# Optimization experiments

Measured on AMD Instinct MI355X. Metric: run time of the kernel, lower is better.

The kernel has to match this reference:

```python
import jax, jax.numpy as jnp
import numpy as np

B = 4        # number of point clouds (equal-sized, batch ids are sorted blocks)
K = 3        # knn_interpolate k
EPS_D = 1e-16
EPS_BN = 1e-5


def setup_inputs() -> dict:
    key = jax.random.key(0)
    ks = jax.random.split(key, 12)
    N_src, N_tgt = 2048, 8192
    C, C_skip = 256, 128
    x = jax.random.normal(ks[0], (B * N_src, C), dtype=jnp.float32)
    pos = jax.random.normal(ks[1], (B * N_src, 3), dtype=jnp.float32)
    x_skip = jax.random.normal(ks[2], (B * N_tgt, C_skip), dtype=jnp.float32)
    pos_skip = jax.random.normal(ks[3], (B * N_tgt, 3), dtype=jnp.float32)
    batch = jnp.repeat(jnp.arange(B, dtype=jnp.int64), N_src)
    batch_skip = jnp.repeat(jnp.arange(B, dtype=jnp.int64), N_tgt)
    d_in = C + C_skip  # 384
    W1 = jax.random.normal(ks[4], (d_in, 256), dtype=jnp.float32) / np.sqrt(d_in)
    b1 = jnp.zeros((256,), dtype=jnp.float32)
    g1 = jnp.ones((256,), dtype=jnp.float32)
    be1 = jnp.zeros((256,), dtype=jnp.float32)
    W2 = jax.random.normal(ks[5], (256, 256), dtype=jnp.float32) / 16.0
    b2 = jnp.zeros((256,), dtype=jnp.float32)
    g2 = jnp.ones((256,), dtype=jnp.float32)
    be2 = jnp.zeros((256,), dtype=jnp.float32)
    return dict(x=x, pos=pos, batch=batch, x_skip=x_skip, pos_skip=pos_skip,
                batch_skip=batch_skip, W1=W1, b1=b1, g1=g1, be1=be1,
                W2=W2, b2=b2, g2=g2, be2=be2)


def _knn_interpolate(x, pos, pos_skip):
    # equal-size clouds: reshape instead of per-batch masking
    C = x.shape[1]
    N = pos.shape[0] // B
    M = pos_skip.shape[0] // B
    ps = pos.reshape(B, N, 3)
    pt = pos_skip.reshape(B, M, 3)
    # squared distances [B, M, N] via |a|^2 + |b|^2 - 2ab
    d2 = (jnp.sum(pt * pt, -1)[:, :, None]
          + jnp.sum(ps * ps, -1)[:, None, :]
          - 2.0 * jnp.einsum('bmd,bnd->bmn', pt, ps))
    neg_d2, idx = jax.lax.top_k(-d2, K)            # idx: [B, M, K]
    w = 1.0 / jnp.maximum(-neg_d2, EPS_D)          # inverse squared distance
    xf = x.reshape(B, N, C)
    feats = xf[jnp.arange(B)[:, None, None], idx]  # [B, M, K, C] irregular gather
    y = jnp.sum(feats * w[..., None], axis=2) / jnp.sum(w, axis=2)[..., None]
    return y.reshape(B * M, C)


def _mlp_block(h, W, b, g, be):
    h = jnp.maximum(h @ W + b, 0.0)                # Linear + ReLU
    mu = jnp.mean(h, axis=0)
    var = jnp.mean((h - mu) ** 2, axis=0)          # biased var (torch BN training)
    return g * (h - mu) / jnp.sqrt(var + EPS_BN) + be


def reference(x, pos, batch, x_skip, pos_skip, batch_skip,
              W1, b1, g1, be1, W2, b2, g2, be2):
    y = _knn_interpolate(x, pos, pos_skip)
    h = jnp.concatenate([y, x_skip], axis=1)       # [B*M, 384]
    h = _mlp_block(h, W1, b1, g1, be1)
    h = _mlp_block(h, W2, b2, g2, be2)
    return h
```

## Files before the change

kernel.cpp:

```cpp
#include <hip/hip_runtime.h>
#include <hip/hip_bf16.h>

typedef __attribute__((ext_vector_type(8))) short short8;
typedef __attribute__((ext_vector_type(4))) short s16x4;
typedef __attribute__((ext_vector_type(4))) int   i32x4;
typedef __attribute__((ext_vector_type(4))) float f32x4;
typedef __attribute__((ext_vector_type(2))) float f32x2;
typedef __attribute__((ext_vector_type(8))) float f32x8;

constexpr int BATCH  = 4;
constexpr int NSRC   = 2048;
constexpr int NTGT   = 8192;
constexpr int C_IN   = 256;
constexpr int C_SKIP = 128;
constexpr int DIN    = 384;
constexpr int HID    = 256;
constexpr int MROWS  = BATCH * NTGT;

constexpr int TGT_PER_BLK = 16;
constexpr int KNN_BLOCKS  = MROWS / TGT_PER_BLK;
constexpr int WT_BLOCKS   = 8;
constexpr int LDS_STRIDE  = 36;

__device__ __forceinline__ short f2bf(float v) {
    __hip_bfloat16 h = __float2bfloat16(v);
    return (short)__builtin_bit_cast(unsigned short, h);
}
__device__ __forceinline__ float bf2f(short s) {
    return __uint_as_float(((unsigned)(unsigned short)s) << 16);
}

__global__ __launch_bounds__(512, 4) void knn_kernel(const float* __restrict__ pos,
                                                     const float* __restrict__ pos_skip,
                                                     const float* __restrict__ W1,
                                                     __hip_bfloat16* __restrict__ W1T,
                                                     i32x4* __restrict__ idxo,
                                                     f32x4* __restrict__ wqo,
                                                     float* __restrict__ stats) {
#pragma clang fp contract(off)
    const int blk = blockIdx.x;
    if (blk >= KNN_BLOCKS) {
        const int e = blk - KNN_BLOCKS;
        if (e < WT_BLOCKS) {
            const int r  = e * 32 + (threadIdx.x >> 4);
            const int c0 = threadIdx.x & 15;
#pragma unroll
            for (int k = 0; k < DIN / 16; ++k) {
                int c = c0 + k * 16;
                W1T[(size_t)r * DIN + c] = __float2bfloat16(W1[(size_t)c * HID + r]);
            }
        } else {
            for (int i = threadIdx.x; i < 4 * HID; i += 512) stats[i] = 0.0f;
        }
        return;
    }
    __shared__ float4 sp[NSRC];
    const int t0 = blk * TGT_PER_BLK;
    const int b  = t0 / NTGT;
    const float* ps = pos + (size_t)b * NSRC * 3;
    for (int j = threadIdx.x; j < NSRC; j += 512) {
        float X = ps[j * 3 + 0], Y = ps[j * 3 + 1], Z = ps[j * 3 + 2];
        float s2 = ((X * X) + (Y * Y)) + (Z * Z);
        sp[j] = make_float4(X, Y, Z, s2);
    }
    __syncthreads();
    const int g  = threadIdx.x >> 5;
    const int s  = threadIdx.x & 31;
    const int tr = t0 + g;
    const float px = pos_skip[tr * 3 + 0], py = pos_skip[tr * 3 + 1], pz = pos_skip[tr * 3 + 2];
    const float pt2 = ((px * px) + (py * py)) + (pz * pz);
    const f32x2 px2 = {px, px}, py2 = {py, py}, pz2 = {pz, pz}, ptv = {pt2, pt2};
    const f32x2 two = {2.0f, 2.0f};
    float bd0 = 3e38f, bd1 = 3e38f, bd2 = 3e38f;
    int   bi0 = 0x7fffffff, bi1 = 0x7fffffff, bi2 = 0x7fffffff;
#pragma unroll 4
    for (int k = 0; k < NSRC / 64; ++k) {
        const int j1 = k * 64 + s;
        const int j2 = j1 + 32;
        float4 sa = sp[j1];
        float4 sb = sp[j2];
        f32x2 vx = {sa.x, sb.x}, vy = {sa.y, sb.y}, vz = {sa.z, sb.z}, vw = {sa.w, sb.w};
        f32x2 dot = ((px2 * vx) + (py2 * vy)) + (pz2 * vz);
        f32x2 d2v = (ptv + vw) - (two * dot);
#pragma unroll
        for (int h = 0; h < 2; ++h) {
            float d2 = h == 0 ? d2v.x : d2v.y;
            int   j  = h == 0 ? j1 : j2;
            bool c0 = d2 < bd0, c1 = d2 < bd1, c2 = d2 < bd2;
            bd2 = c1 ? bd1 : (c2 ? d2 : bd2);  bi2 = c1 ? bi1 : (c2 ? j : bi2);
            bd1 = c0 ? bd0 : (c1 ? d2 : bd1);  bi1 = c0 ? bi0 : (c1 ? j : bi1);
            bd0 = c0 ? d2  : bd0;              bi0 = c0 ? j  : bi0;
        }
    }
#pragma unroll
    for (int m = 1; m <= 16; m <<= 1) {
        float od0 = __shfl_xor(bd0, m), od1 = __shfl_xor(bd1, m), od2 = __shfl_xor(bd2, m);
        int   oi0 = __shfl_xor(bi0, m), oi1 = __shfl_xor(bi1, m), oi2 = __shfl_xor(bi2, m);
#pragma unroll
        for (int e = 0; e < 3; ++e) {
            float d = e == 0 ? od0 : (e == 1 ? od1 : od2);
            int   i = e == 0 ? oi0 : (e == 1 ? oi1 : oi2);
            bool c0 = (d < bd0) || (d == bd0 && i < bi0);
            bool c1 = (d < bd1) || (d == bd1 && i < bi1);
            bool c2 = (d < bd2) || (d == bd2 && i < bi2);
            bd2 = c1 ? bd1 : (c2 ? d : bd2);  bi2 = c1 ? bi1 : (c2 ? i : bi2);
            bd1 = c0 ? bd0 : (c1 ? d : bd1);  bi1 = c0 ? bi0 : (c1 ? i : bi1);
            bd0 = c0 ? d   : bd0;             bi0 = c0 ? i  : bi0;
        }
    }
    if (s == 0) {
        float w0 = 1.0f / fmaxf(bd0, 1e-16f);
        float w1 = 1.0f / fmaxf(bd1, 1e-16f);
        float w2 = 1.0f / fmaxf(bd2, 1e-16f);
        float inv = 1.0f / ((w0 + w1) + w2);
        idxo[tr] = i32x4{bi0, bi1, bi2, 0};
        wqo[tr]  = f32x4{w0 * inv, w1 * inv, w2 * inv, 0.0f};
    }
}

__global__ __launch_bounds__(256, 1) void zs_kernel(const float* __restrict__ x,
                                                    const float* __restrict__ xs,
                                                    const __hip_bfloat16* __restrict__ W1T,
                                                    __hip_bfloat16* __restrict__ Z,
                                                    __hip_bfloat16* __restrict__ S) {
    __shared__ short As[128 * LDS_STRIDE];
    const int blk = blockIdx.x;
    const float* A;
    __hip_bfloat16* out;
    int K, koff, m0;
    if (blk < 64) { A = x;  out = Z; K = 256; koff = 0;   m0 = blk * 128; }
    else          { A = xs; out = S; K = 128; koff = 256; m0 = (blk - 64) * 128; }
    const int t = threadIdx.x;
    const int wid = t >> 6, lane = t & 63;
    const int wr = wid & 1, wcq = wid >> 1;
    const int l15 = lane & 15, l4 = lane >> 4;
    const int arow = t >> 1, ac16 = (t & 1) * 16;
    const short* Wsh = (const short*)W1T;
    f32x4 acc[4][8] = {};
    for (int kt = 0; kt < K / 32; ++kt) {
        const float* src = A + (size_t)(m0 + arow) * K + kt * 32 + ac16;
        float4 f0 = *(const float4*)(src);
        float4 f1 = *(const float4*)(src + 4);
        float4 f2 = *(const float4*)(src + 8);
        float4 f3 = *(const float4*)(src + 12);
        short8 s0 = {f2bf(f0.x), f2bf(f0.y), f2bf(f0.z), f2bf(f0.w),
                     f2bf(f1.x), f2bf(f1.y), f2bf(f1.z), f2bf(f1.w)};
        short8 s1 = {f2bf(f2.x), f2bf(f2.y), f2bf(f2.z), f2bf(f2.w),
                     f2bf(f3.x), f2bf(f3.y), f2bf(f3.z), f2bf(f3.w)};
        __syncthreads();
        *(short8*)(&As[arow * LDS_STRIDE + ac16])     = s0;
        *(short8*)(&As[arow * LDS_STRIDE + ac16 + 8]) = s1;
        __syncthreads();
        short8 af[4], bfr[8];
#pragma unroll
        for (int mi = 0; mi < 4; ++mi)
            af[mi] = *(const short8*)(&As[(wr * 64 + mi * 16 + l15) * LDS_STRIDE + l4 * 8]);
#pragma unroll
        for (int ni = 0; ni < 8; ++ni)
            bfr[ni] = *(const short8*)(Wsh + (size_t)(wcq * 128 + ni * 16 + l15) * DIN + koff + kt * 32 + l4 * 8);
#pragma unroll
        for (int mi = 0; mi < 4; ++mi)
#pragma unroll
            for (int ni = 0; ni < 8; ++ni)
                acc[mi][ni] = __builtin_amdgcn_mfma_f32_16x16x32_bf16(af[mi], bfr[ni], acc[mi][ni], 0, 0, 0);
    }
#pragma unroll
    for (int mi = 0; mi < 4; ++mi)
#pragma unroll
        for (int r = 0; r < 4; ++r) {
            int rowg = m0 + wr * 64 + mi * 16 + l4 * 4 + r;
#pragma unroll
            for (int ni = 0; ni < 8; ++ni) {
                int col = wcq * 128 + ni * 16 + l15;
                out[(size_t)rowg * HID + col] = __float2bfloat16(acc[mi][ni][r]);
            }
        }
}

__global__ __launch_bounds__(256) void interp_kernel(const __hip_bfloat16* __restrict__ Z,
                                                     const __hip_bfloat16* __restrict__ S,
                                                     const i32x4* __restrict__ idxo,
                                                     const f32x4* __restrict__ wqo,
                                                     const float* __restrict__ b1,
                                                     __hip_bfloat16* __restrict__ H1) {
    const int t = blockIdx.x * 256 + threadIdx.x;
    const int r = t >> 5;
    const int c = (t & 31) * 8;
    i32x4 id = idxo[r];
    f32x4 wq = wqo[r];
    const int zb = (r >> 13) << 11;
    const short* Zs = (const short*)Z;
    short8 z0 = *(const short8*)(Zs + (size_t)(zb + id.x) * HID + c);
    short8 z1 = *(const short8*)(Zs + (size_t)(zb + id.y) * HID + c);
    short8 z2 = *(const short8*)(Zs + (size_t)(zb + id.z) * HID + c);
    short8 sv = *(const short8*)((const short*)S + (size_t)r * HID + c);
    f32x4 b0 = *(const f32x4*)(b1 + c);
    f32x4 b4 = *(const f32x4*)(b1 + c + 4);
    short8 ho;
#pragma unroll
    for (int e = 0; e < 8; ++e) {
        float bb = e < 4 ? b0[e & 3] : b4[e & 3];
        float v = wq.x * bf2f(z0[e]) + wq.y * bf2f(z1[e]) + wq.z * bf2f(z2[e])
                  + bf2f(sv[e]) + bb;
        ho[e] = f2bf(fmaxf(v, 0.0f));
    }
    *(short8*)((short*)H1 + (size_t)r * HID + c) = ho;
}

__global__ __launch_bounds__(256) void stats1_kernel(const __hip_bfloat16* __restrict__ H1,
                                                     float* __restrict__ sum1,
                                                     float* __restrict__ sq1) {
    const int c  = threadIdx.x;
    const int r0 = blockIdx.x * (MROWS / 128);
    const short* Hs = (const short*)H1;
    float s = 0.0f, q = 0.0f;
#pragma unroll 8
    for (int r = 0; r < MROWS / 128; ++r) {
        float v = bf2f(Hs[(size_t)(r0 + r) * HID + c]);
        s += v;
        q += v * v;
    }
    atomicAdd(&sum1[c], s);
    atomicAdd(&sq1[c], q);
}

template <int K>
__global__ __launch_bounds__(256, 1) void gemm_kernel(const __hip_bfloat16* __restrict__ A,
                                                      const __hip_bfloat16* __restrict__ WT,
                                                      const float* __restrict__ bias,
                                                      __hip_bfloat16* __restrict__ outp,
                                                      float* __restrict__ colsum,
                                                      float* __restrict__ colsq) {
    __shared__ short As[128 * LDS_STRIDE];
    const int t = threadIdx.x;
    const int m0 = blockIdx.x * 128;
    const int wid = t >> 6, lane = t & 63;
    const int wr = wid & 1, wcq = wid >> 1;
    const int l15 = lane & 15, l4 = lane >> 4;
    const int arow = t >> 1, acol8 = (t & 1) * 8;
    f32x4 acc[4][8] = {};
    const short* Ash = (const short*)A;
    const short* Wsh = (const short*)WT;
    for (int kt = 0; kt < K / 32; ++kt) {
        short8 v0 = *(const short8*)(Ash + (size_t)(m0 + arow) * K + kt * 32 + acol8);
        short8 v1 = *(const short8*)(Ash + (size_t)(m0 + arow) * K + kt * 32 + acol8 + 16);
        __syncthreads();
        *(short8*)(&As[arow * LDS_STRIDE + acol8]) = v0;
        *(short8*)(&As[arow * LDS_STRIDE + acol8 + 16]) = v1;
        __syncthreads();
        short8 af[4], bfr[8];
#pragma unroll
        for (int mi = 0; mi < 4; ++mi)
            af[mi] = *(const short8*)(&As[(wr * 64 + mi * 16 + l15) * LDS_STRIDE + l4 * 8]);
#pragma unroll
        for (int ni = 0; ni < 8; ++ni)
            bfr[ni] = *(const short8*)(Wsh + (size_t)(wcq * 128 + ni * 16 + l15) * K + kt * 32 + l4 * 8);
#pragma unroll
        for (int mi = 0; mi < 4; ++mi)
#pragma unroll
            for (int ni = 0; ni < 8; ++ni)
                acc[mi][ni] = __builtin_amdgcn_mfma_f32_16x16x32_bf16(af[mi], bfr[ni], acc[mi][ni], 0, 0, 0);
    }
    float bv[8];
    int col[8];
#pragma unroll
    for (int ni = 0; ni < 8; ++ni) {
        col[ni] = wcq * 128 + ni * 16 + l15;
        bv[ni] = bias[col[ni]];
    }
    float csum[8] = {}, csq[8] = {};
#pragma unroll
    for (int mi = 0; mi < 4; ++mi) {
#pragma unroll
        for (int r = 0; r < 4; ++r) {
            int rowg = m0 + wr * 64 + mi * 16 + l4 * 4 + r;
#pragma unroll
            for (int ni = 0; ni < 8; ++ni) {
                float v = fmaxf(acc[mi][ni][r] + bv[ni], 0.0f);
                outp[(size_t)rowg * HID + col[ni]] = __float2bfloat16(v);
                csum[ni] += v;
                csq[ni] += v * v;
            }
        }
    }
#pragma unroll
    for (int ni = 0; ni < 8; ++ni) {
        float sv = csum[ni], q = csq[ni];
        sv += __shfl_xor(sv, 16); sv += __shfl_xor(sv, 32);
        q  += __shfl_xor(q, 16);  q  += __shfl_xor(q, 32);
        if (l4 == 0) {
            atomicAdd(&colsum[col[ni]], sv);
            atomicAdd(&colsq[col[ni]], q);
        }
    }
}

__global__ __launch_bounds__(256) void foldw2_kernel(const float* __restrict__ W2,
                                                     const float* __restrict__ b2,
                                                     const float* __restrict__ sum1,
                                                     const float* __restrict__ sq1,
                                                     const float* __restrict__ g1,
                                                     const float* __restrict__ be1,
                                                     __hip_bfloat16* __restrict__ W2T,
                                                     float* __restrict__ bias2f) {
    __shared__ float red[256];
    const int n = blockIdx.x, k = threadIdx.x;
    float mu  = sum1[k] * (1.0f / MROWS);
    float var = sq1[k] * (1.0f / MROWS) - mu * mu;
    float scv = g1[k] / sqrtf(var + 1e-5f);
    float shv = be1[k] - mu * scv;
    float v = W2[(size_t)k * HID + n];
    W2T[(size_t)n * HID + k] = __float2bfloat16(scv * v);
    red[k] = shv * v;
    __syncthreads();
    for (int s = 128; s > 0; s >>= 1) {
        if (k < s) red[k] += red[k + s];
        __syncthreads();
    }
    if (k == 0) bias2f[n] = b2[n] + red[0];
}

__global__ __launch_bounds__(256) void bn2_kernel(const __hip_bfloat16* __restrict__ h2,
                                                  const float* __restrict__ sum2,
                                                  const float* __restrict__ sq2,
                                                  const float* __restrict__ g2,
                                                  const float* __restrict__ be2,
                                                  float* __restrict__ out) {
    __shared__ float lsc[HID], lsh[HID];
    {
        int c = threadIdx.x;
        float mu  = sum2[c] * (1.0f / MROWS);
        float var = sq2[c] * (1.0f / MROWS) - mu * mu;
        float scv = g2[c] / sqrtf(var + 1e-5f);
        lsc[c] = scv;
        lsh[c] = be2[c] - mu * scv;
    }
    __syncthreads();
    int idx = blockIdx.x * blockDim.x + threadIdx.x;
    const int total = MROWS * HID / 8;
    for (; idx < total; idx += gridDim.x * blockDim.x) {
        short8 v = *(const short8*)(h2 + (size_t)idx * 8);
        int c = (idx * 8) & (HID - 1);
        f32x8 o;
#pragma unroll
        for (int e = 0; e < 8; ++e) {
            float f = bf2f(v[e]);
            o[e] = lsc[c + e] * f + lsh[c + e];
        }
        *(f32x8*)(out + (size_t)idx * 8) = o;
    }
}

extern "C" void kernel_launch(void* const* d_in, const int* in_sizes, int n_in,
                              void* d_out, int out_size, void* d_ws, size_t ws_size,
                              hipStream_t stream) {
    const float* x    = (const float*)d_in[0];
    const float* pos  = (const float*)d_in[1];
    const float* xs   = (const float*)d_in[3];
    const float* poss = (const float*)d_in[4];
    const float* W1   = (const float*)d_in[6];
    const float* b1   = (const float*)d_in[7];
    const float* g1   = (const float*)d_in[8];
    const float* be1  = (const float*)d_in[9];
    const float* W2   = (const float*)d_in[10];
    const float* b2   = (const float*)d_in[11];
    const float* g2   = (const float*)d_in[12];
    const float* be2  = (const float*)d_in[13];

    char* ws = (char*)d_ws;
    size_t off = 0;
    auto alloc = [&](size_t bytes) -> void* {
        void* p = ws + off;
        off += (bytes + 255) & ~(size_t)255;
        return p;
    };
    __hip_bfloat16* W1T   = (__hip_bfloat16*)alloc((size_t)HID * DIN * 2);
    __hip_bfloat16* W2T   = (__hip_bfloat16*)alloc((size_t)HID * HID * 2);
    float*          stats = (float*)alloc(4 * HID * sizeof(float));
    float *sum1 = stats, *sq1 = stats + HID, *sum2 = stats + 2 * HID, *sq2 = stats + 3 * HID;
    float*          bias2f = (float*)alloc(HID * sizeof(float));
    i32x4*          idxo  = (i32x4*)alloc((size_t)MROWS * 16);
    f32x4*          wqo   = (f32x4*)alloc((size_t)MROWS * 16);
    __hip_bfloat16* Z     = (__hip_bfloat16*)alloc((size_t)BATCH * NSRC * HID * 2);
    __hip_bfloat16* S     = (__hip_bfloat16*)alloc((size_t)MROWS * HID * 2);
    __hip_bfloat16* H1    = (__hip_bfloat16*)alloc((size_t)MROWS * HID * 2);
    __hip_bfloat16* H2    = S;

    knn_kernel<<<KNN_BLOCKS + WT_BLOCKS + 1, 512, 0, stream>>>(pos, poss, W1, W1T, idxo, wqo, stats);
    zs_kernel<<<64 + MROWS / 128, 256, 0, stream>>>(x, xs, W1T, Z, S);
    interp_kernel<<<MROWS * 32 / 256, 256, 0, stream>>>(Z, S, idxo, wqo, b1, H1);
    stats1_kernel<<<128, 256, 0, stream>>>(H1, sum1, sq1);
    foldw2_kernel<<<HID, 256, 0, stream>>>(W2, b2, sum1, sq1, g1, be1, W2T, bias2f);
    gemm_kernel<HID><<<MROWS / 128, 256, 0, stream>>>(H1, W2T, bias2f, H2, sum2, sq2);
    bn2_kernel<<<1024, 256, 0, stream>>>(H2, sum2, sq2, g2, be2, (float*)d_out);
}
```

Before: 141.3 us.

## Fuse BN1 stats into interp kernel and halve GEMM row tiles

Folds the layer-1 column sum/sum-of-squares into the interpolation kernel, which now handles four row chunks per thread and reduces them through LDS before issuing atomics. This removes the separate stats1 pass that re-read H1. Both the Z/S GEMM and the second GEMM now use 64-row tiles with launch bounds allowing two blocks per CU, doubling the grid for better occupancy. The price is more redundant weight-fragment loads per output row.

```diff
diff --git a/kernel.cpp b/kernel.cpp
--- a/kernel.cpp
+++ b/kernel.cpp
@@ -2,7 +2,6 @@
 #include <hip/hip_bf16.h>
 
 typedef __attribute__((ext_vector_type(8))) short short8;
-typedef __attribute__((ext_vector_type(4))) short s16x4;
 typedef __attribute__((ext_vector_type(4))) int   i32x4;
 typedef __attribute__((ext_vector_type(4))) float f32x4;
 typedef __attribute__((ext_vector_type(2))) float f32x2;
@@ -118,57 +117,52 @@
     }
 }
 
-__global__ __launch_bounds__(256, 1) void zs_kernel(const float* __restrict__ x,
+__global__ __launch_bounds__(256, 2) void zs_kernel(const float* __restrict__ x,
                                                     const float* __restrict__ xs,
                                                     const __hip_bfloat16* __restrict__ W1T,
                                                     __hip_bfloat16* __restrict__ Z,
                                                     __hip_bfloat16* __restrict__ S) {
-    __shared__ short As[128 * LDS_STRIDE];
+    __shared__ short As[64 * LDS_STRIDE];
     const int blk = blockIdx.x;
     const float* A;
     __hip_bfloat16* out;
     int K, koff, m0;
-    if (blk < 64) { A = x;  out = Z; K = 256; koff = 0;   m0 = blk * 128; }
-    else          { A = xs; out = S; K = 128; koff = 256; m0 = (blk - 64) * 128; }
+    if (blk < 128) { A = x;  out = Z; K = 256; koff = 0;   m0 = blk * 64; }
+    else           { A = xs; out = S; K = 128; koff = 256; m0 = (blk - 128) * 64; }
     const int t = threadIdx.x;
     const int wid = t >> 6, lane = t & 63;
     const int wr = wid & 1, wcq = wid >> 1;
     const int l15 = lane & 15, l4 = lane >> 4;
-    const int arow = t >> 1, ac16 = (t & 1) * 16;
+    const int arow = t >> 2, ac8 = (t & 3) * 8;
     const short* Wsh = (const short*)W1T;
-    f32x4 acc[4][8] = {};
+    f32x4 acc[2][8] = {};
     for (int kt = 0; kt < K / 32; ++kt) {
-        const float* src = A + (size_t)(m0 + arow) * K + kt * 32 + ac16;
+        const float* src = A + (size_t)(m0 + arow) * K + kt * 32 + ac8;
         float4 f0 = *(const float4*)(src);
         float4 f1 = *(const float4*)(src + 4);
-        float4 f2 = *(const float4*)(src + 8);
-        float4 f3 = *(const float4*)(src + 12);
         short8 s0 = {f2bf(f0.x), f2bf(f0.y), f2bf(f0.z), f2bf(f0.w),
                      f2bf(f1.x), f2bf(f1.y), f2bf(f1.z), f2bf(f1.w)};
-        short8 s1 = {f2bf(f2.x), f2bf(f2.y), f2bf(f2.z), f2bf(f2.w),
-                     f2bf(f3.x), f2bf(f3.y), f2bf(f3.z), f2bf(f3.w)};
-        __syncthreads();
-        *(short8*)(&As[arow * LDS_STRIDE + ac16])     = s0;
-        *(short8*)(&As[arow * LDS_STRIDE + ac16 + 8]) = s1;
-        __syncthreads();
-        short8 af[4], bfr[8];
-#pragma unroll
-        for (int mi = 0; mi < 4; ++mi)
-            af[mi] = *(const short8*)(&As[(wr * 64 + mi * 16 + l15) * LDS_STRIDE + l4 * 8]);
+        __syncthreads();
+        *(short8*)(&As[arow * LDS_STRIDE + ac8]) = s0;
+        __syncthreads();
+        short8 af[2], bfr[8];
+#pragma unroll
+        for (int mi = 0; mi < 2; ++mi)
+            af[mi] = *(const short8*)(&As[(wr * 32 + mi * 16 + l15) * LDS_STRIDE + l4 * 8]);
 #pragma unroll
         for (int ni = 0; ni < 8; ++ni)
             bfr[ni] = *(const short8*)(Wsh + (size_t)(wcq * 128 + ni * 16 + l15) * DIN + koff + kt * 32 + l4 * 8);
 #pragma unroll
-        for (int mi = 0; mi < 4; ++mi)
+        for (int mi = 0; mi < 2; ++mi)
 #pragma unroll
             for (int ni = 0; ni < 8; ++ni)
                 acc[mi][ni] = __builtin_amdgcn_mfma_f32_16x16x32_bf16(af[mi], bfr[ni], acc[mi][ni], 0, 0, 0);
     }
 #pragma unroll
-    for (int mi = 0; mi < 4; ++mi)
+    for (int mi = 0; mi < 2; ++mi)
 #pragma unroll
         for (int r = 0; r < 4; ++r) {
-            int rowg = m0 + wr * 64 + mi * 16 + l4 * 4 + r;
+            int rowg = m0 + wr * 32 + mi * 16 + l4 * 4 + r;
 #pragma unroll
             for (int ni = 0; ni < 8; ++ni) {
                 int col = wcq * 128 + ni * 16 + l15;
@@ -182,81 +176,85 @@
                                                      const i32x4* __restrict__ idxo,
                                                      const f32x4* __restrict__ wqo,
                                                      const float* __restrict__ b1,
-                                                     __hip_bfloat16* __restrict__ H1) {
-    const int t = blockIdx.x * 256 + threadIdx.x;
-    const int r = t >> 5;
-    const int c = (t & 31) * 8;
-    i32x4 id = idxo[r];
-    f32x4 wq = wqo[r];
-    const int zb = (r >> 13) << 11;
-    const short* Zs = (const short*)Z;
-    short8 z0 = *(const short8*)(Zs + (size_t)(zb + id.x) * HID + c);
-    short8 z1 = *(const short8*)(Zs + (size_t)(zb + id.y) * HID + c);
-    short8 z2 = *(const short8*)(Zs + (size_t)(zb + id.z) * HID + c);
-    short8 sv = *(const short8*)((const short*)S + (size_t)r * HID + c);
-    f32x4 b0 = *(const f32x4*)(b1 + c);
-    f32x4 b4 = *(const f32x4*)(b1 + c + 4);
-    short8 ho;
-#pragma unroll
-    for (int e = 0; e < 8; ++e) {
-        float bb = e < 4 ? b0[e & 3] : b4[e & 3];
-        float v = wq.x * bf2f(z0[e]) + wq.y * bf2f(z1[e]) + wq.z * bf2f(z2[e])
-                  + bf2f(sv[e]) + bb;
-        ho[e] = f2bf(fmaxf(v, 0.0f));
-    }
-    *(short8*)((short*)H1 + (size_t)r * HID + c) = ho;
-}
-
-__global__ __launch_bounds__(256) void stats1_kernel(const __hip_bfloat16* __restrict__ H1,
+                                                     __hip_bfloat16* __restrict__ H1,
                                                      float* __restrict__ sum1,
                                                      float* __restrict__ sq1) {
-    const int c  = threadIdx.x;
-    const int r0 = blockIdx.x * (MROWS / 128);
-    const short* Hs = (const short*)H1;
-    float s = 0.0f, q = 0.0f;
-#pragma unroll 8
-    for (int r = 0; r < MROWS / 128; ++r) {
-        float v = bf2f(Hs[(size_t)(r0 + r) * HID + c]);
-        s += v;
-        q += v * v;
-    }
-    atomicAdd(&sum1[c], s);
-    atomicAdd(&sq1[c], q);
-}
-
-template <int K>
-__global__ __launch_bounds__(256, 1) void gemm_kernel(const __hip_bfloat16* __restrict__ A,
-                                                      const __hip_bfloat16* __restrict__ WT,
-                                                      const float* __restrict__ bias,
-                                                      __hip_bfloat16* __restrict__ outp,
-                                                      float* __restrict__ colsum,
-                                                      float* __restrict__ colsq) {
-    __shared__ short As[128 * LDS_STRIDE];
+    __shared__ float ls[8][HID], lq[8][HID];
     const int t = threadIdx.x;
-    const int m0 = blockIdx.x * 128;
+    const int cbase = (t & 31) * 8;
+    f32x4 b0 = *(const f32x4*)(b1 + cbase);
+    f32x4 b4 = *(const f32x4*)(b1 + cbase + 4);
+    const short* Zs = (const short*)Z;
+    float cs[8] = {}, cq[8] = {};
+#pragma unroll
+    for (int i = 0; i < 4; ++i) {
+        const int gid = blockIdx.x * 1024 + i * 256 + t;
+        const int r = gid >> 5;
+        const int c = cbase;
+        i32x4 id = idxo[r];
+        f32x4 wq = wqo[r];
+        const int zb = (r >> 13) << 11;
+        short8 z0 = *(const short8*)(Zs + (size_t)(zb + id.x) * HID + c);
+        short8 z1 = *(const short8*)(Zs + (size_t)(zb + id.y) * HID + c);
+        short8 z2 = *(const short8*)(Zs + (size_t)(zb + id.z) * HID + c);
+        short8 sv = *(const short8*)((const short*)S + (size_t)r * HID + c);
+        short8 ho;
+#pragma unroll
+        for (int e = 0; e < 8; ++e) {
+            float bb = e < 4 ? b0[e & 3] : b4[e & 3];
+            float v = wq.x * bf2f(z0[e]) + wq.y * bf2f(z1[e]) + wq.z * bf2f(z2[e])
+                      + bf2f(sv[e]) + bb;
+            v = fmaxf(v, 0.0f);
+            ho[e] = f2bf(v);
+            cs[e] += v;
+            cq[e] += v * v;
+        }
+        *(short8*)((short*)H1 + (size_t)r * HID + c) = ho;
+    }
+    const int grp = t >> 5;
+    *(f32x4*)(&ls[grp][cbase])     = f32x4{cs[0], cs[1], cs[2], cs[3]};
+    *(f32x4*)(&ls[grp][cbase + 4]) = f32x4{cs[4], cs[5], cs[6], cs[7]};
+    *(f32x4*)(&lq[grp][cbase])     = f32x4{cq[0], cq[1], cq[2], cq[3]};
+    *(f32x4*)(&lq[grp][cbase + 4]) = f32x4{cq[4], cq[5], cq[6], cq[7]};
+    __syncthreads();
+    float s_ = 0.0f, q_ = 0.0f;
+#pragma unroll
+    for (int g2 = 0; g2 < 8; ++g2) { s_ += ls[g2][t]; q_ += lq[g2][t]; }
+    atomicAdd(&sum1[t], s_);
+    atomicAdd(&sq1[t], q_);
+}
+
+__global__ __launch_bounds__(256, 2) void gemm2_kernel(const __hip_bfloat16* __restrict__ A,
+                                                       const __hip_bfloat16* __restrict__ WT,
+                                                       const float* __restrict__ bias,
+                                                       __hip_bfloat16* __restrict__ outp,
+                                                       float* __restrict__ colsum,
+                                                       float* __restrict__ colsq) {
+    __shared__ short As[64 * LDS_STRIDE];
+    const int t = threadIdx.x;
+    const int m0 = blockIdx.x * 64;
     const int wid = t >> 6, lane = t & 63;
     const int wr = wid & 1, wcq = wid >> 1;
     const int l15 = lane & 15, l4 = lane >> 4;
-    const int arow = t >> 1, acol8 = (t & 1) * 8;
-    f32x4 acc[4][8] = {};
+    const int arow = t >> 2, ac8 = (t & 3) * 8;
+    f32x4 acc[2][8] = {};
     const short* Ash = (const short*)A;
     const short* Wsh = (const short*)WT;
+    constexpr int K = HID;
     for (int kt = 0; kt < K / 32; ++kt) {
-        short8 v0 = *(const short8*)(Ash + (size_t)(m0 + arow) * K + kt * 32 + acol8);
-        short8 v1 = *(const short8*)(Ash + (size_t)(m0 + arow) * K + kt * 32 + acol8 + 16);
-        __syncthreads();
-        *(short8*)(&As[arow * LDS_STRIDE + acol8]) = v0;
-        *(short8*)(&As[arow * LDS_STRIDE + acol8 + 16]) = v1;
-        __syncthreads();
-        short8 af[4], bfr[8];
-#pragma unroll
-        for (int mi = 0; mi < 4; ++mi)
-            af[mi] = *(const short8*)(&As[(wr * 64 + mi * 16 + l15) * LDS_STRIDE + l4 * 8]);
+        short8 v0 = *(const short8*)(Ash + (size_t)(m0 + arow) * K + kt * 32 + ac8);
+        __syncthreads();
+        *(short8*)(&As[arow * LDS_STRIDE + ac8]) = v0;
+        __syncthreads();
+        short8 af[2], bfr[8];
+#pragma unroll
+        for (int mi = 0; mi < 2; ++mi)
+            af[mi] = *(const short8*)(&As[(wr * 32 + mi * 16 + l15) * LDS_STRIDE + l4 * 8]);
 #pragma unroll
         for (int ni = 0; ni < 8; ++ni)
             bfr[ni] = *(const short8*)(Wsh + (size_t)(wcq * 128 + ni * 16 + l15) * K + kt * 32 + l4 * 8);
 #pragma unroll
-        for (int mi = 0; mi < 4; ++mi)
+        for (int mi = 0; mi < 2; ++mi)
 #pragma unroll
             for (int ni = 0; ni < 8; ++ni)
                 acc[mi][ni] = __builtin_amdgcn_mfma_f32_16x16x32_bf16(af[mi], bfr[ni], acc[mi][ni], 0, 0, 0);
@@ -270,10 +268,10 @@
     }
     float csum[8] = {}, csq[8] = {};
 #pragma unroll
-    for (int mi = 0; mi < 4; ++mi) {
+    for (int mi = 0; mi < 2; ++mi) {
 #pragma unroll
         for (int r = 0; r < 4; ++r) {
-            int rowg = m0 + wr * 64 + mi * 16 + l4 * 4 + r;
+            int rowg = m0 + wr * 32 + mi * 16 + l4 * 4 + r;
 #pragma unroll
             for (int ni = 0; ni < 8; ++ni) {
                 float v = fmaxf(acc[mi][ni][r] + bv[ni], 0.0f);
@@ -387,10 +385,9 @@
     __hip_bfloat16* H2    = S;
 
     knn_kernel<<<KNN_BLOCKS + WT_BLOCKS + 1, 512, 0, stream>>>(pos, poss, W1, W1T, idxo, wqo, stats);
-    zs_kernel<<<64 + MROWS / 128, 256, 0, stream>>>(x, xs, W1T, Z, S);
-    interp_kernel<<<MROWS * 32 / 256, 256, 0, stream>>>(Z, S, idxo, wqo, b1, H1);
-    stats1_kernel<<<128, 256, 0, stream>>>(H1, sum1, sq1);
+    zs_kernel<<<128 + MROWS / 64, 256, 0, stream>>>(x, xs, W1T, Z, S);
+    interp_kernel<<<MROWS * 32 / 1024, 256, 0, stream>>>(Z, S, idxo, wqo, b1, H1, sum1, sq1);
     foldw2_kernel<<<HID, 256, 0, stream>>>(W2, b2, sum1, sq1, g1, be1, W2T, bias2f);
-    gemm_kernel<HID><<<MROWS / 128, 256, 0, stream>>>(H1, W2T, bias2f, H2, sum2, sq2);
+    gemm2_kernel<<<MROWS / 64, 256, 0, stream>>>(H1, W2T, bias2f, H2, sum2, sq2);
     bn2_kernel<<<1024, 256, 0, stream>>>(H2, sum2, sq2, g2, be2, (float*)d_out);
 }
```

Result: slower. 164.5 us (+16.4%).

## Fuse second BatchNorm into GEMM2 via grid-wide barrier, drop H2 round-trip

Applied to the files above, without the earlier changes.

The second GEMM no longer writes a bf16 intermediate. It keeps its accumulators in registers, accumulates column statistics, then waits on a software grid barrier (an atomic counter reset in the knn kernel) for all 256 blocks. After the barrier it reads the final sums, applies the BN2 scale and shift, and writes the fp32 output directly. This removes the bn2 kernel launch and the write and re-read of H2. It relies on all 256 blocks being co-resident (one per CU at launch bounds 256,1), which risks deadlock if that does not hold, and blocks spin while waiting.

```diff
diff --git a/kernel.cpp b/kernel.cpp
--- a/kernel.cpp
+++ b/kernel.cpp
@@ -2,7 +2,6 @@
 #include <hip/hip_bf16.h>
 
 typedef __attribute__((ext_vector_type(8))) short short8;
-typedef __attribute__((ext_vector_type(4))) short s16x4;
 typedef __attribute__((ext_vector_type(4))) int   i32x4;
 typedef __attribute__((ext_vector_type(4))) float f32x4;
 typedef __attribute__((ext_vector_type(2))) float f32x2;
@@ -21,6 +20,7 @@
 constexpr int KNN_BLOCKS  = MROWS / TGT_PER_BLK;
 constexpr int WT_BLOCKS   = 8;
 constexpr int LDS_STRIDE  = 36;
+constexpr int G2_BLOCKS   = MROWS / 128;
 
 __device__ __forceinline__ short f2bf(float v) {
     __hip_bfloat16 h = __float2bfloat16(v);
@@ -36,7 +36,8 @@
                                                      __hip_bfloat16* __restrict__ W1T,
                                                      i32x4* __restrict__ idxo,
                                                      f32x4* __restrict__ wqo,
-                                                     float* __restrict__ stats) {
+                                                     float* __restrict__ stats,
+                                                     int* __restrict__ barrier_ct) {
 #pragma clang fp contract(off)
     const int blk = blockIdx.x;
     if (blk >= KNN_BLOCKS) {
@@ -51,6 +52,7 @@
             }
         } else {
             for (int i = threadIdx.x; i < 4 * HID; i += 512) stats[i] = 0.0f;
+            if (threadIdx.x == 0) *barrier_ct = 0;
         }
         return;
     }
@@ -224,13 +226,15 @@
     atomicAdd(&sq1[c], q);
 }
 
-template <int K>
-__global__ __launch_bounds__(256, 1) void gemm_kernel(const __hip_bfloat16* __restrict__ A,
-                                                      const __hip_bfloat16* __restrict__ WT,
-                                                      const float* __restrict__ bias,
-                                                      __hip_bfloat16* __restrict__ outp,
-                                                      float* __restrict__ colsum,
-                                                      float* __restrict__ colsq) {
+__global__ __launch_bounds__(256, 1) void gemm2_kernel(const __hip_bfloat16* __restrict__ A,
+                                                       const __hip_bfloat16* __restrict__ WT,
+                                                       const float* __restrict__ bias,
+                                                       float* __restrict__ out,
+                                                       float* __restrict__ colsum,
+                                                       float* __restrict__ colsq,
+                                                       const float* __restrict__ g2,
+                                                       const float* __restrict__ be2,
+                                                       int* __restrict__ barrier_ct) {
     __shared__ short As[128 * LDS_STRIDE];
     const int t = threadIdx.x;
     const int m0 = blockIdx.x * 128;
@@ -241,6 +245,7 @@
     f32x4 acc[4][8] = {};
     const short* Ash = (const short*)A;
     const short* Wsh = (const short*)WT;
+    constexpr int K = HID;
     for (int kt = 0; kt < K / 32; ++kt) {
         short8 v0 = *(const short8*)(Ash + (size_t)(m0 + arow) * K + kt * 32 + acol8);
         short8 v1 = *(const short8*)(Ash + (size_t)(m0 + arow) * K + kt * 32 + acol8 + 16);
@@ -270,19 +275,15 @@
     }
     float csum[8] = {}, csq[8] = {};
 #pragma unroll
-    for (int mi = 0; mi < 4; ++mi) {
-#pragma unroll
-        for (int r = 0; r < 4; ++r) {
-            int rowg = m0 + wr * 64 + mi * 16 + l4 * 4 + r;
+    for (int mi = 0; mi < 4; ++mi)
+#pragma unroll
+        for (int r = 0; r < 4; ++r)
 #pragma unroll
             for (int ni = 0; ni < 8; ++ni) {
                 float v = fmaxf(acc[mi][ni][r] + bv[ni], 0.0f);
-                outp[(size_t)rowg * HID + col[ni]] = __float2bfloat16(v);
                 csum[ni] += v;
                 csq[ni] += v * v;
             }
-        }
-    }
 #pragma unroll
     for (int ni = 0; ni < 8; ++ni) {
         float sv = csum[ni], q = csq[ni];
@@ -293,6 +294,36 @@
             atomicAdd(&colsq[col[ni]], q);
         }
     }
+    __syncthreads();
+    if (t == 0) {
+        __threadfence();
+        __hip_atomic_fetch_add(barrier_ct, 1, __ATOMIC_ACQ_REL, __HIP_MEMORY_SCOPE_AGENT);
+        while (__hip_atomic_load(barrier_ct, __ATOMIC_ACQUIRE, __HIP_MEMORY_SCOPE_AGENT) < G2_BLOCKS) {}
+        __threadfence();
+    }
+    __syncthreads();
+    float sc2[8], sh2[8];
+#pragma unroll
+    for (int ni = 0; ni < 8; ++ni) {
+        float sm = __hip_atomic_load(&colsum[col[ni]], __ATOMIC_ACQUIRE, __HIP_MEMORY_SCOPE_AGENT);
+        float qq = __hip_atomic_load(&colsq[col[ni]],  __ATOMIC_ACQUIRE, __HIP_MEMORY_SCOPE_AGENT);
+        float mu  = sm * (1.0f / MROWS);
+        float var = qq * (1.0f / MROWS) - mu * mu;
+        float scv = g2[col[ni]] / sqrtf(var + 1e-5f);
+        sc2[ni] = scv;
+        sh2[ni] = be2[col[ni]] - mu * scv;
+    }
+#pragma unroll
+    for (int mi = 0; mi < 4; ++mi)
+#pragma unroll
+        for (int r = 0; r < 4; ++r) {
+            int rowg = m0 + wr * 64 + mi * 16 + l4 * 4 + r;
+#pragma unroll
+            for (int ni = 0; ni < 8; ++ni) {
+                float v = fmaxf(acc[mi][ni][r] + bv[ni], 0.0f);
+                out[(size_t)rowg * HID + col[ni]] = sc2[ni] * v + sh2[ni];
+            }
+        }
 }
 
 __global__ __launch_bounds__(256) void foldw2_kernel(const float* __restrict__ W2,
@@ -320,37 +351,6 @@
     if (k == 0) bias2f[n] = b2[n] + red[0];
 }
 
-__global__ __launch_bounds__(256) void bn2_kernel(const __hip_bfloat16* __restrict__ h2,
-                                                  const float* __restrict__ sum2,
-                                                  const float* __restrict__ sq2,
-                                                  const float* __restrict__ g2,
-                                                  const float* __restrict__ be2,
-                                                  float* __restrict__ out) {
-    __shared__ float lsc[HID], lsh[HID];
-    {
-        int c = threadIdx.x;
-        float mu  = sum2[c] * (1.0f / MROWS);
-        float var = sq2[c] * (1.0f / MROWS) - mu * mu;
-        float scv = g2[c] / sqrtf(var + 1e-5f);
-        lsc[c] = scv;
-        lsh[c] = be2[c] - mu * scv;
-    }
-    __syncthreads();
-    int idx = blockIdx.x * blockDim.x + threadIdx.x;
-    const int total = MROWS * HID / 8;
-    for (; idx < total; idx += gridDim.x * blockDim.x) {
-        short8 v = *(const short8*)(h2 + (size_t)idx * 8);
-        int c = (idx * 8) & (HID - 1);
-        f32x8 o;
-#pragma unroll
-        for (int e = 0; e < 8; ++e) {
-            float f = bf2f(v[e]);
-            o[e] = lsc[c + e] * f + lsh[c + e];
-        }
-        *(f32x8*)(out + (size_t)idx * 8) = o;
-    }
-}
-
 extern "C" void kernel_launch(void* const* d_in, const int* in_sizes, int n_in,
                               void* d_out, int out_size, void* d_ws, size_t ws_size,
                               hipStream_t stream) {
@@ -379,18 +379,19 @@
     float*          stats = (float*)alloc(4 * HID * sizeof(float));
     float *sum1 = stats, *sq1 = stats + HID, *sum2 = stats + 2 * HID, *sq2 = stats + 3 * HID;
     float*          bias2f = (float*)alloc(HID * sizeof(float));
+    int*            barrier_ct = (int*)alloc(256);
     i32x4*          idxo  = (i32x4*)alloc((size_t)MROWS * 16);
     f32x4*          wqo   = (f32x4*)alloc((size_t)MROWS * 16);
     __hip_bfloat16* Z     = (__hip_bfloat16*)alloc((size_t)BATCH * NSRC * HID * 2);
     __hip_bfloat16* S     = (__hip_bfloat16*)alloc((size_t)MROWS * HID * 2);
     __hip_bfloat16* H1    = (__hip_bfloat16*)alloc((size_t)MROWS * HID * 2);
-    __hip_bfloat16* H2    = S;
-
-    knn_kernel<<<KNN_BLOCKS + WT_BLOCKS + 1, 512, 0, stream>>>(pos, poss, W1, W1T, idxo, wqo, stats);
+
+    knn_kernel<<<KNN_BLOCKS + WT_BLOCKS + 1, 512, 0, stream>>>(pos, poss, W1, W1T, idxo, wqo,
+                                                               stats, barrier_ct);
     zs_kernel<<<64 + MROWS / 128, 256, 0, stream>>>(x, xs, W1T, Z, S);
     interp_kernel<<<MROWS * 32 / 256, 256, 0, stream>>>(Z, S, idxo, wqo, b1, H1);
     stats1_kernel<<<128, 256, 0, stream>>>(H1, sum1, sq1);
     foldw2_kernel<<<HID, 256, 0, stream>>>(W2, b2, sum1, sq1, g1, be1, W2T, bias2f);
-    gemm_kernel<HID><<<MROWS / 128, 256, 0, stream>>>(H1, W2T, bias2f, H2, sum2, sq2);
-    bn2_kernel<<<1024, 256, 0, stream>>>(H2, sum2, sq2, g2, be2, (float*)d_out);
-}
+    gemm2_kernel<<<G2_BLOCKS, 256, 0, stream>>>(H1, W2T, bias2f, (float*)d_out, sum2, sq2,
+                                                g2, be2, barrier_ct);
+}
```

Measured after the change: 268.6 us. 1.9x slower.

## Two-pass KNN: value-only min3 via med3, then index pass filtered by threshold

Applied to the files above, without the earlier changes.

The KNN inner loop now keeps all 64 per-lane distances in registers and first runs a value-only top-3 using fmin/fmed3, which avoids index selects. A wave-wide butterfly merge then finds the global third-smallest distance. A second pass runs the full index-tracking insertion only for candidates under that threshold, skipping it wave-uniformly otherwise. Holding 64 distances in registers raises register pressure, so launch bounds drop from 4 to 2 waves per EU, which lowers occupancy.

```diff
diff --git a/kernel.cpp b/kernel.cpp
--- a/kernel.cpp
+++ b/kernel.cpp
@@ -2,7 +2,6 @@
 #include <hip/hip_bf16.h>
 
 typedef __attribute__((ext_vector_type(8))) short short8;
-typedef __attribute__((ext_vector_type(4))) short s16x4;
 typedef __attribute__((ext_vector_type(4))) int   i32x4;
 typedef __attribute__((ext_vector_type(4))) float f32x4;
 typedef __attribute__((ext_vector_type(2))) float f32x2;
@@ -30,7 +29,7 @@
     return __uint_as_float(((unsigned)(unsigned short)s) << 16);
 }
 
-__global__ __launch_bounds__(512, 4) void knn_kernel(const float* __restrict__ pos,
+__global__ __launch_bounds__(512, 2) void knn_kernel(const float* __restrict__ pos,
                                                      const float* __restrict__ pos_skip,
                                                      const float* __restrict__ W1,
                                                      __hip_bfloat16* __restrict__ W1T,
@@ -71,9 +70,10 @@
     const float pt2 = ((px * px) + (py * py)) + (pz * pz);
     const f32x2 px2 = {px, px}, py2 = {py, py}, pz2 = {pz, pz}, ptv = {pt2, pt2};
     const f32x2 two = {2.0f, 2.0f};
-    float bd0 = 3e38f, bd1 = 3e38f, bd2 = 3e38f;
-    int   bi0 = 0x7fffffff, bi1 = 0x7fffffff, bi2 = 0x7fffffff;
-#pragma unroll 4
+
+    float dreg[64];
+    float a0 = 3e38f, a1 = 3e38f, a2 = 3e38f;
+#pragma unroll
     for (int k = 0; k < NSRC / 64; ++k) {
         const int j1 = k * 64 + s;
         const int j2 = j1 + 32;
@@ -82,10 +82,37 @@
         f32x2 vx = {sa.x, sb.x}, vy = {sa.y, sb.y}, vz = {sa.z, sb.z}, vw = {sa.w, sb.w};
         f32x2 dot = ((px2 * vx) + (py2 * vy)) + (pz2 * vz);
         f32x2 d2v = (ptv + vw) - (two * dot);
+        dreg[2 * k]     = d2v.x;
+        dreg[2 * k + 1] = d2v.y;
 #pragma unroll
         for (int h = 0; h < 2; ++h) {
-            float d2 = h == 0 ? d2v.x : d2v.y;
-            int   j  = h == 0 ? j1 : j2;
+            float d = h == 0 ? d2v.x : d2v.y;
+            float n0 = fminf(a0, d);
+            float n1 = __builtin_amdgcn_fmed3f(a0, a1, d);
+            float n2 = fminf(a2, fmaxf(a1, d));
+            a0 = n0; a1 = n1; a2 = n2;
+        }
+    }
+#pragma unroll
+    for (int m = 1; m <= 16; m <<= 1) {
+        float oa = __shfl_xor(a0, m), ob = __shfl_xor(a1, m), oc = __shfl_xor(a2, m);
+        float minb = fminf(a1, ob);
+        float maxa = fmaxf(a0, oa);
+        float maxb = fmaxf(a1, ob);
+        float minc = fminf(a2, oc);
+        float n0 = fminf(a0, oa);
+        float n1 = __builtin_amdgcn_fmed3f(a0, oa, minb);
+        float n2 = __builtin_amdgcn_fmed3f(minb, maxa, fminf(maxb, minc));
+        a0 = n0; a1 = n1; a2 = n2;
+    }
+
+    float bd0 = 3e38f, bd1 = 3e38f, bd2 = 3e38f;
+    int   bi0 = 0x7fffffff, bi1 = 0x7fffffff, bi2 = 0x7fffffff;
+#pragma unroll
+    for (int i = 0; i < 64; ++i) {
+        float d2 = dreg[i];
+        if (__any(d2 <= a2)) {
+            const int j = (i >> 1) * 64 + ((i & 1) << 5) + s;
             bool c0 = d2 < bd0, c1 = d2 < bd1, c2 = d2 < bd2;
             bd2 = c1 ? bd1 : (c2 ? d2 : bd2);  bi2 = c1 ? bi1 : (c2 ? j : bi2);
             bd1 = c0 ? bd0 : (c1 ? d2 : bd1);  bi1 = c0 ? bi0 : (c1 ? j : bi1);
```

Result: faster. 134.7 us (-4.7%).
